# Kernel optimization log

Measured on AMD Instinct MI355X. Metric: run time of the kernel, lower is better.

Reference implementation:

```python
import jax, jax.numpy as jnp
import numpy as np

D_MODEL = 1024
NHEAD = 16
HEAD_DIM = D_MODEL // NHEAD
WINDOW = 256


def setup_inputs() -> dict:
    key = jax.random.key(0)
    kx, kq, kk, kv, ko = jax.random.split(key, 5)
    B, S = 2, 2048
    scale = 1.0 / np.sqrt(D_MODEL)
    x = jax.random.normal(kx, (B, S, D_MODEL), dtype=jnp.float32)
    Wq = jax.random.normal(kq, (D_MODEL, D_MODEL), dtype=jnp.float32) * scale
    Wk = jax.random.normal(kk, (D_MODEL, D_MODEL), dtype=jnp.float32) * scale
    Wv = jax.random.normal(kv, (D_MODEL, D_MODEL), dtype=jnp.float32) * scale
    Wo = jax.random.normal(ko, (D_MODEL, D_MODEL), dtype=jnp.float32) * scale
    return {"x": x, "Wq": Wq, "Wk": Wk, "Wv": Wv, "Wo": Wo}


def _sliding_window_mask(seq_len):
    # additive mask: 0 where (q - window + 1) <= k <= q, -inf elsewhere
    pos = jnp.arange(seq_len)
    qpos = pos[:, None]
    kpos = pos[None, :]
    valid = (kpos >= qpos - WINDOW + 1) & (kpos <= qpos)
    return jnp.where(valid, 0.0, -jnp.inf).astype(jnp.float32)


def reference(x, Wq, Wk, Wv, Wo):
    B, S, D = x.shape
    # projections (nn.Linear: x @ W.T; weights here stored as [out,in] equiv -> use x @ W.T)
    q = jnp.einsum('bsd,ed->bse', x, Wq)
    k = jnp.einsum('bsd,ed->bse', x, Wk)
    v = jnp.einsum('bsd,ed->bse', x, Wv)
    q = q.reshape(B, S, NHEAD, HEAD_DIM).transpose(0, 2, 1, 3)  # [B,H,S,Dh]
    k = k.reshape(B, S, NHEAD, HEAD_DIM).transpose(0, 2, 1, 3)
    v = v.reshape(B, S, NHEAD, HEAD_DIM).transpose(0, 2, 1, 3)
    mask = _sliding_window_mask(S)  # [S,S]
    scale = 1.0 / np.sqrt(HEAD_DIM)
    scores = jnp.einsum('bhqd,bhkd->bhqk', q, k) * scale + mask
    attn = jax.nn.softmax(scores, axis=-1)
    out = jnp.einsum('bhqk,bhkd->bhqd', attn, v)  # [B,H,S,Dh]
    out = out.transpose(0, 2, 1, 3).reshape(B, S, D)
    return jnp.einsum('bsd,ed->bse', out, Wo)
```

## Files before the change

### kernel.cpp

```cpp
#include <hip/hip_runtime.h>
#include <stdint.h>

#define S_LEN   2048
#define BATCH   2
#define DM      1024
#define NHEADS  16
#define HD      64
#define WIN     256
#define MROWS   (BATCH * S_LEN)
#define NX      (MROWS * DM)
#define NW      (DM * DM)

typedef unsigned short u16;
typedef unsigned int   u32;

using short8  = __attribute__((ext_vector_type(8))) short;
using floatx4 = __attribute__((ext_vector_type(4))) float;

__device__ __forceinline__ float bf2f(u16 u) {
    union { u32 u; float f; } v; v.u = ((u32)u) << 16; return v.f;
}
__device__ __forceinline__ u16 f2bf(float f) {
    union { float f; u32 u; } v; v.f = f;
    u32 u = v.u;
    u += 0x7fffu + ((u >> 16) & 1u);
    return (u16)(u >> 16);
}

__device__ __forceinline__ void load_lds16(const void* g, void* l) {
    __builtin_amdgcn_global_load_lds(
        (__attribute__((address_space(1))) void*)(uintptr_t)g,
        (__attribute__((address_space(3))) void*)(unsigned int)(uintptr_t)l,
        16, 0, 0);
}

__global__ __launch_bounds__(256) void detect_mode(const u16* x, int* flag) {
    __shared__ int sbad;
    int t = threadIdx.x;
    if (t == 0) sbad = 0;
    __syncthreads();
    int bad = 0;
    for (int i = t; i < 4096; i += 256) {
        float v = bf2f(x[i]);
        if (!(fabsf(v) < 1e6f)) bad = 1;
    }
    if (bad) atomicOr(&sbad, 1);
    __syncthreads();
    if (t == 0) flag[0] = sbad;
}

__global__ __launch_bounds__(256) void normalize_inputs(
        const void* x, const void* wq, const void* wk, const void* wv, const void* wo,
        u16* xb, u16* wcat, u16* wob, const int* flag) {
    if (flag[0] == 0) return;
    const int total = NX + 4 * NW;
    for (int i = blockIdx.x * blockDim.x + threadIdx.x; i < total;
         i += gridDim.x * blockDim.x) {
        const void* src; u16* dst; int li;
        if (i < NX)              { src = x;  dst = xb;            li = i; }
        else if (i < NX + NW)    { src = wq; dst = wcat;          li = i - NX; }
        else if (i < NX + 2*NW)  { src = wk; dst = wcat + NW;     li = i - NX - NW; }
        else if (i < NX + 3*NW)  { src = wv; dst = wcat + 2*NW;   li = i - NX - 2*NW; }
        else                     { src = wo; dst = wob;           li = i - NX - 3*NW; }
        dst[li] = f2bf(((const float*)src)[li]);
    }
}

#define BM 128
#define BN 128
#define BK 32

__global__ __launch_bounds__(256) void gemm_lds(
        const u16* __restrict__ Araw, const u16* __restrict__ Anorm,
        const u16* __restrict__ B0, const u16* __restrict__ B1,
        const u16* __restrict__ B2, const u16* __restrict__ Bnorm,
        void* __restrict__ C, int M, int N, int K,
        const int* __restrict__ flag, int final_out) {
    __shared__ __align__(16) u16 sA[BM * BK];
    __shared__ __align__(16) u16 sB[BN * BK];

    const int mode = flag[0];
    const int tid  = threadIdx.x;
    const int lane = tid & 63, wave = tid >> 6;
    const int m0  = blockIdx.x * BM;
    const int n0g = blockIdx.y * BN;
    const int third = n0g >> 10;
    const u16* A = mode ? Anorm : Araw;
    const u16* B = mode ? (Bnorm + (size_t)third * NW)
                        : (third == 0 ? B0 : (third == 1 ? B1 : B2));
    const int n0 = n0g - third * 1024;

    const int srow = lane >> 2;
    const int fsw  = ((lane >> 2) & 3) ^ ((lane >> 4) & 1);
    const int scol = ((lane & 3) ^ fsw) * 8;
    const u16* gA = A + (size_t)(m0 + wave * 16 + srow) * K + scol;
    const u16* gB = B + (size_t)(n0 + wave * 16 + srow) * K + scol;
    u16* lA = sA + wave * 16 * BK;
    u16* lB = sB + wave * 16 * BK;
    const size_t rstep = (size_t)64 * K;

    const int n16 = lane & 15, quad = lane >> 4;
    const int m_off = (wave >> 1) * 64, n_off = (wave & 1) * 64;
    const int fr   = (n16 & 3) ^ ((n16 >> 2) & 1);
    const int cswz = ((quad ^ fr) & 3) * 8;

    floatx4 acc[4][4] = {};

    for (int k0 = 0; k0 < K; k0 += BK) {
        load_lds16(gA + k0,         lA);
        load_lds16(gA + k0 + rstep, lA + 64 * BK);
        load_lds16(gB + k0,         lB);
        load_lds16(gB + k0 + rstep, lB + 64 * BK);
        __syncthreads();
        short8 af[4], bfr[4];
        #pragma unroll
        for (int i = 0; i < 4; ++i)
            af[i] = *(const short8*)&sA[(m_off + i * 16 + n16) * BK + cswz];
        #pragma unroll
        for (int j = 0; j < 4; ++j)
            bfr[j] = *(const short8*)&sB[(n_off + j * 16 + n16) * BK + cswz];
        #pragma unroll
        for (int i = 0; i < 4; ++i) {
            #pragma unroll
            for (int j = 0; j < 4; ++j)
                acc[i][j] = __builtin_amdgcn_mfma_f32_16x16x32_bf16(
                    af[i], bfr[j], acc[i][j], 0, 0, 0);
        }
        __syncthreads();
    }

    const int outmode = final_out ? mode : 0;
    const float oscale = (!final_out && n0g < 1024) ? 0.125f : 1.0f;
    #pragma unroll
    for (int i = 0; i < 4; ++i) {
        #pragma unroll
        for (int j = 0; j < 4; ++j) {
            #pragma unroll
            for (int r = 0; r < 4; ++r) {
                int row = m0 + m_off + i * 16 + quad * 4 + r;
                int col = n0g + n_off + j * 16 + n16;
                size_t idx = (size_t)row * N + col;
                float v = acc[i][j][r] * oscale;
                if (outmode) ((float*)C)[idx] = v;
                else         ((u16*)C)[idx]   = f2bf(v);
            }
        }
    }
}

#define KSTG 384
#define KPAD 72
#define VPAD 394

__global__ __launch_bounds__(512) void attn_mfma(
        const u16* __restrict__ QKV, u16* __restrict__ O) {
    __shared__ __align__(16) u16 sK[KSTG][KPAD];
    __shared__ __align__(16) u16 sVt[64][VPAD];
    __shared__ __align__(16) u16 sP[8][2][16][40];

    const int bh = blockIdx.x;
    const int b  = bh >> 4, h = bh & 15;
    const int q0 = blockIdx.y * 128;
    const int kb0 = q0 - (WIN - 1);
    const int tid = threadIdx.x;
    const u16* base = QKV + (size_t)b * S_LEN * 3072;

    for (int i = tid; i < KSTG * 8; i += 512) {
        int row = i >> 3, seg = i & 7;
        int kg = kb0 + row;
        uint4 kv = {0u, 0u, 0u, 0u}, vv = {0u, 0u, 0u, 0u};
        if (kg >= 0 && kg < S_LEN) {
            const u16* rp = base + (size_t)kg * 3072 + h * 64 + seg * 8;
            kv = *(const uint4*)(rp + 1024);
            vv = *(const uint4*)(rp + 2048);
        }
        *(uint4*)&sK[row][seg * 8] = kv;
        const u16* vp = (const u16*)&vv;
        #pragma unroll
        for (int t2 = 0; t2 < 8; ++t2) sVt[seg * 8 + t2][row] = vp[t2];
    }
    __syncthreads();

    const int wave = tid >> 6, lane = tid & 63;
    const int n16 = lane & 15, quad = lane >> 4;
    const int sqb = q0 + wave * 16;
    const int sq_r0 = sqb + quad * 4;

    const u16* qrow = base + (size_t)(sqb + n16) * 3072 + h * 64;
    short8 aq0 = *(const short8*)(qrow + quad * 8);
    short8 aq1 = *(const short8*)(qrow + 32 + quad * 8);

    floatx4 o0 = {0.f,0.f,0.f,0.f}, o1 = o0, o2 = o0, o3 = o0;
    float m[4] = {-1e30f, -1e30f, -1e30f, -1e30f};
    float l[4] = {0.f, 0.f, 0.f, 0.f};
    const int c0 = wave >> 1;

    for (int cc = 0; cc < 9; ++cc) {
        const int krel = (c0 + cc) * 32;
        short8 bk00 = *(const short8*)&sK[krel + n16][quad * 8];
        short8 bk01 = *(const short8*)&sK[krel + n16][32 + quad * 8];
        short8 bk10 = *(const short8*)&sK[krel + 16 + n16][quad * 8];
        short8 bk11 = *(const short8*)&sK[krel + 16 + n16][32 + quad * 8];
        floatx4 z = {0.f, 0.f, 0.f, 0.f};
        floatx4 s0 = __builtin_amdgcn_mfma_f32_16x16x32_bf16(aq0, bk00, z, 0, 0, 0);
        s0 = __builtin_amdgcn_mfma_f32_16x16x32_bf16(aq1, bk01, s0, 0, 0, 0);
        floatx4 s1 = __builtin_amdgcn_mfma_f32_16x16x32_bf16(aq0, bk10, z, 0, 0, 0);
        s1 = __builtin_amdgcn_mfma_f32_16x16x32_bf16(aq1, bk11, s1, 0, 0, 0);

        const int kg0 = kb0 + krel + n16;
        const int kg1 = kg0 + 16;
        float alpha[4], p0[4], p1[4];
        #pragma unroll
        for (int r = 0; r < 4; ++r) {
            int sq = sq_r0 + r;
            int lo = sq - (WIN - 1); if (lo < 0) lo = 0;
            float v0 = (kg0 >= lo && kg0 <= sq) ? s0[r] : -1e30f;
            float v1 = (kg1 >= lo && kg1 <= sq) ? s1[r] : -1e30f;
            float mc = fmaxf(v0, v1);
            mc = fmaxf(mc, __shfl_xor(mc, 1));
            mc = fmaxf(mc, __shfl_xor(mc, 2));
            mc = fmaxf(mc, __shfl_xor(mc, 4));
            mc = fmaxf(mc, __shfl_xor(mc, 8));
            float mn = fmaxf(m[r], mc);
            alpha[r] = __expf(m[r] - mn);
            m[r] = mn;
            p0[r] = __expf(v0 - mn);
            p1[r] = __expf(v1 - mn);
            float rs = p0[r] + p1[r];
            rs += __shfl_xor(rs, 1);
            rs += __shfl_xor(rs, 2);
            rs += __shfl_xor(rs, 4);
            rs += __shfl_xor(rs, 8);
            l[r] = l[r] * alpha[r] + rs;
        }
        #pragma unroll
        for (int r = 0; r < 4; ++r) {
            o0[r] *= alpha[r]; o1[r] *= alpha[r];
            o2[r] *= alpha[r]; o3[r] *= alpha[r];
        }
        u16* pw = &sP[wave][cc & 1][0][0];
        #pragma unroll
        for (int r = 0; r < 4; ++r) {
            pw[(quad * 4 + r) * 40 + n16]      = f2bf(p0[r]);
            pw[(quad * 4 + r) * 40 + 16 + n16] = f2bf(p1[r]);
        }
        asm volatile("s_waitcnt lgkmcnt(0)" ::: "memory");
        short8 pa  = *(const short8*)&pw[n16 * 40 + quad * 8];
        short8 bv0 = *(const short8*)&sVt[n16]     [krel + quad * 8];
        short8 bv1 = *(const short8*)&sVt[16 + n16][krel + quad * 8];
        short8 bv2 = *(const short8*)&sVt[32 + n16][krel + quad * 8];
        short8 bv3 = *(const short8*)&sVt[48 + n16][krel + quad * 8];
        o0 = __builtin_amdgcn_mfma_f32_16x16x32_bf16(pa, bv0, o0, 0, 0, 0);
        o1 = __builtin_amdgcn_mfma_f32_16x16x32_bf16(pa, bv1, o1, 0, 0, 0);
        o2 = __builtin_amdgcn_mfma_f32_16x16x32_bf16(pa, bv2, o2, 0, 0, 0);
        o3 = __builtin_amdgcn_mfma_f32_16x16x32_bf16(pa, bv3, o3, 0, 0, 0);
    }

    #pragma unroll
    for (int r = 0; r < 4; ++r) {
        float rl = 1.0f / l[r];
        size_t ro = ((size_t)(b * S_LEN + sq_r0 + r)) * DM + h * 64 + n16;
        O[ro]      = f2bf(o0[r] * rl);
        O[ro + 16] = f2bf(o1[r] * rl);
        O[ro + 32] = f2bf(o2[r] * rl);
        O[ro + 48] = f2bf(o3[r] * rl);
    }
}

extern "C" void kernel_launch(void* const* d_in, const int* in_sizes, int n_in,
                              void* d_out, int out_size, void* d_ws, size_t ws_size,
                              hipStream_t stream) {
    char* ws = (char*)d_ws;
    int* flag = (int*)ws;
    u16* xb   = (u16*)(ws + 1024);
    u16* wcat = xb   + (size_t)NX;
    u16* wob  = wcat + (size_t)3 * NW;
    u16* qkv  = wob  + (size_t)NW;
    u16* ob   = qkv  + (size_t)MROWS * 3 * DM;

    const u16* xr  = (const u16*)d_in[0];
    const u16* wqr = (const u16*)d_in[1];
    const u16* wkr = (const u16*)d_in[2];
    const u16* wvr = (const u16*)d_in[3];
    const u16* wor = (const u16*)d_in[4];

    detect_mode<<<1, 256, 0, stream>>>(xr, flag);
    normalize_inputs<<<4096, 256, 0, stream>>>(
        d_in[0], d_in[1], d_in[2], d_in[3], d_in[4], xb, wcat, wob, flag);
    gemm_lds<<<dim3(MROWS / BM, 3072 / BN), 256, 0, stream>>>(
        xr, xb, wqr, wkr, wvr, wcat, qkv, MROWS, 3 * DM, DM, flag, 0);
    attn_mfma<<<dim3(BATCH * NHEADS, S_LEN / 128), 512, 0, stream>>>(qkv, ob);
    gemm_lds<<<dim3(MROWS / BM, DM / BN), 256, 0, stream>>>(
        ob, ob, wor, wor, wor, wob, d_out, MROWS, DM, DM, flag, 1);
}
```

Measured before the change: 190.9 us.

## Double-buffer GEMM LDS tiles, template tile width, drop swizzle, shrink convert grid

The GEMM now keeps two LDS buffers and issues the next K-slice's global-to-LDS loads before computing on the current one. This removes one barrier per iteration and overlaps load latency with MFMA work. The kernel is templated on tile width so the output projection uses 128x64 tiles, which doubles its block count for better occupancy on the smaller N=1024 GEMM. The LDS XOR swizzle is removed, which may bring back bank conflicts, and the conversion kernel grid is cut to 1024 blocks.

```diff
diff --git a/kernel.cpp b/kernel.cpp
--- a/kernel.cpp
+++ b/kernel.cpp
@@ -67,23 +67,24 @@
 }
 
 #define BM 128
-#define BN 128
 #define BK 32
 
+template<int TBN>
 __global__ __launch_bounds__(256) void gemm_lds(
         const u16* __restrict__ Araw, const u16* __restrict__ Anorm,
         const u16* __restrict__ B0, const u16* __restrict__ B1,
         const u16* __restrict__ B2, const u16* __restrict__ Bnorm,
         void* __restrict__ C, int M, int N, int K,
         const int* __restrict__ flag, int final_out) {
-    __shared__ __align__(16) u16 sA[BM * BK];
-    __shared__ __align__(16) u16 sB[BN * BK];
+    constexpr int NF = TBN / 32;
+    __shared__ __align__(16) u16 sA[2][BM * BK];
+    __shared__ __align__(16) u16 sB[2][TBN * BK];
 
     const int mode = flag[0];
     const int tid  = threadIdx.x;
     const int lane = tid & 63, wave = tid >> 6;
     const int m0  = blockIdx.x * BM;
-    const int n0g = blockIdx.y * BN;
+    const int n0g = blockIdx.y * TBN;
     const int third = n0g >> 10;
     const u16* A = mode ? Anorm : Araw;
     const u16* B = mode ? (Bnorm + (size_t)third * NW)
@@ -91,42 +92,46 @@
     const int n0 = n0g - third * 1024;
 
     const int srow = lane >> 2;
-    const int fsw  = ((lane >> 2) & 3) ^ ((lane >> 4) & 1);
-    const int scol = ((lane & 3) ^ fsw) * 8;
+    const int scol = (lane & 3) * 8;
     const u16* gA = A + (size_t)(m0 + wave * 16 + srow) * K + scol;
     const u16* gB = B + (size_t)(n0 + wave * 16 + srow) * K + scol;
-    u16* lA = sA + wave * 16 * BK;
-    u16* lB = sB + wave * 16 * BK;
     const size_t rstep = (size_t)64 * K;
+    const int lofs = wave * 16 * BK;
 
     const int n16 = lane & 15, quad = lane >> 4;
-    const int m_off = (wave >> 1) * 64, n_off = (wave & 1) * 64;
-    const int fr   = (n16 & 3) ^ ((n16 >> 2) & 1);
-    const int cswz = ((quad ^ fr) & 3) * 8;
-
-    floatx4 acc[4][4] = {};
-
-    for (int k0 = 0; k0 < K; k0 += BK) {
+    const int m_off = (wave >> 1) * 64, n_off = (wave & 1) * (TBN / 2);
+
+    floatx4 acc[4][NF] = {};
+    const int NIT = K / BK;
+
+    auto issue = [&](int k0, int buf) {
+        u16* lA = sA[buf] + lofs;
+        u16* lB = sB[buf] + lofs;
         load_lds16(gA + k0,         lA);
         load_lds16(gA + k0 + rstep, lA + 64 * BK);
-        load_lds16(gB + k0,         lB);
-        load_lds16(gB + k0 + rstep, lB + 64 * BK);
+        load_lds16(gB + k0, lB);
+        if (TBN == 128) load_lds16(gB + k0 + rstep, lB + 64 * BK);
+    };
+
+    issue(0, 0);
+    for (int it = 0; it < NIT; ++it) {
+        const int cur = it & 1;
         __syncthreads();
-        short8 af[4], bfr[4];
+        if (it + 1 < NIT) issue((it + 1) * BK, 1 - cur);
+        short8 af[4], bfr[NF];
         #pragma unroll
         for (int i = 0; i < 4; ++i)
-            af[i] = *(const short8*)&sA[(m_off + i * 16 + n16) * BK + cswz];
-        #pragma unroll
-        for (int j = 0; j < 4; ++j)
-            bfr[j] = *(const short8*)&sB[(n_off + j * 16 + n16) * BK + cswz];
+            af[i] = *(const short8*)&sA[cur][(m_off + i * 16 + n16) * BK + quad * 8];
+        #pragma unroll
+        for (int j = 0; j < NF; ++j)
+            bfr[j] = *(const short8*)&sB[cur][(n_off + j * 16 + n16) * BK + quad * 8];
         #pragma unroll
         for (int i = 0; i < 4; ++i) {
             #pragma unroll
-            for (int j = 0; j < 4; ++j)
+            for (int j = 0; j < NF; ++j)
                 acc[i][j] = __builtin_amdgcn_mfma_f32_16x16x32_bf16(
                     af[i], bfr[j], acc[i][j], 0, 0, 0);
         }
-        __syncthreads();
     }
 
     const int outmode = final_out ? mode : 0;
@@ -134,7 +139,7 @@
     #pragma unroll
     for (int i = 0; i < 4; ++i) {
         #pragma unroll
-        for (int j = 0; j < 4; ++j) {
+        for (int j = 0; j < NF; ++j) {
             #pragma unroll
             for (int r = 0; r < 4; ++r) {
                 int row = m0 + m_off + i * 16 + quad * 4 + r;
@@ -285,11 +290,11 @@
     const u16* wor = (const u16*)d_in[4];
 
     detect_mode<<<1, 256, 0, stream>>>(xr, flag);
-    normalize_inputs<<<4096, 256, 0, stream>>>(
+    normalize_inputs<<<1024, 256, 0, stream>>>(
         d_in[0], d_in[1], d_in[2], d_in[3], d_in[4], xb, wcat, wob, flag);
-    gemm_lds<<<dim3(MROWS / BM, 3072 / BN), 256, 0, stream>>>(
+    gemm_lds<128><<<dim3(MROWS / BM, 3072 / 128), 256, 0, stream>>>(
         xr, xb, wqr, wkr, wvr, wcat, qkv, MROWS, 3 * DM, DM, flag, 0);
     attn_mfma<<<dim3(BATCH * NHEADS, S_LEN / 128), 512, 0, stream>>>(qkv, ob);
-    gemm_lds<<<dim3(MROWS / BM, DM / BN), 256, 0, stream>>>(
+    gemm_lds<64><<<dim3(MROWS / BM, DM / 64), 256, 0, stream>>>(
         ob, ob, wor, wor, wor, wob, d_out, MROWS, DM, DM, flag, 1);
 }
```

Result: faster. 173.9 us (-8.9%).
